# Optimization experiments

Hardware: AMD Instinct MI355X
Metric: run time of the kernel (lower is better)

## Reference

```python
import jax, jax.numpy as jnp
import numpy as np

IMG_H = IMG_W = 14
HEADS = 8
HEAD_DIM = 32
INNER = HEADS * HEAD_DIM  # 256
IN_CH = 384
OUT_CH = 768
HIDDEN = 4 * IN_CH  # 1536
SCALE = HEAD_DIM ** -0.5
EPS = 1e-5


def _relative_index(h, w):
    # static numpy computation, identical to the torch buffer
    yy, xx = np.meshgrid(np.arange(h), np.arange(w), indexing='ij')
    coords = np.stack([yy.ravel(), xx.ravel()])            # [2, N]
    rel = coords[:, :, None] - coords[:, None, :]          # [2, N, N]
    rel[0] += h - 1
    rel[1] += w - 1
    rel[0] *= 2 * w - 1
    return (rel[0] + rel[1]).reshape(-1)                   # [N*N]


def _maxpool3s2p1(x):
    # torch MaxPool2d(3, 2, 1): pad with -inf
    return jax.lax.reduce_window(
        x, -jnp.inf, jax.lax.max,
        window_dimensions=(1, 1, 3, 3),
        window_strides=(1, 1, 2, 2),
        padding=((0, 0), (0, 0), (1, 1), (1, 1)))


def _layernorm(x, g, b):
    mu = jnp.mean(x, axis=-1, keepdims=True)
    var = jnp.mean(jnp.square(x - mu), axis=-1, keepdims=True)
    return (x - mu) * jax.lax.rsqrt(var + EPS) * g + b


def setup_inputs() -> dict:
    key = jax.random.key(0)
    ks = jax.random.split(key, 12)
    s = 0.02
    return {
        'x': jax.random.normal(ks[0], (64, IN_CH, 28, 28), jnp.float32),
        'W_qkv': jax.random.normal(ks[1], (IN_CH, 3 * INNER), jnp.float32) * s,
        'bias_table': jax.random.normal(ks[2], ((2 * IMG_H - 1) * (2 * IMG_W - 1), HEADS), jnp.float32) * s,
        'W_out': jax.random.normal(ks[3], (INNER, OUT_CH), jnp.float32) * s,
        'b_out': jnp.zeros((OUT_CH,), jnp.float32),
        'ln1_g': jnp.ones((IN_CH,), jnp.float32),
        'ln1_b': jnp.zeros((IN_CH,), jnp.float32),
        'ln2_g': jnp.ones((OUT_CH,), jnp.float32),
        'ln2_b': jnp.zeros((OUT_CH,), jnp.float32),
        'W_fc1': jax.random.normal(ks[4], (OUT_CH, HIDDEN), jnp.float32) * s,
        'b_fc1': jnp.zeros((HIDDEN,), jnp.float32),
        'W_fc2': jax.random.normal(ks[5], (HIDDEN, OUT_CH), jnp.float32) * s,
        'b_fc2': jnp.zeros((OUT_CH,), jnp.float32),
        'W_proj': jax.random.normal(ks[6], (OUT_CH, IN_CH), jnp.float32) * s,
    }


def reference(x, W_qkv, bias_table, W_out, b_out, ln1_g, ln1_b, ln2_g, ln2_b,
              W_fc1, b_fc1, W_fc2, b_fc2, W_proj):
    B = x.shape[0]
    N = IMG_H * IMG_W
    rel_idx = jnp.asarray(_relative_index(IMG_H, IMG_W))   # [N*N]

    # --- downsample branch ---
    xp = _maxpool3s2p1(x)                                  # [B, Cin, 14, 14]
    proj = jnp.einsum('bchw,oc->bohw', xp, W_proj)         # 1x1 conv, no bias

    # --- attention branch ---
    xa = _maxpool3s2p1(x)                                  # [B, Cin, 14, 14]
    tokens = xa.reshape(B, IN_CH, N).transpose(0, 2, 1)    # [B, N, Cin]
    tokens = _layernorm(tokens, ln1_g, ln1_b)
    qkv = tokens @ W_qkv                                   # [B, N, 3*INNER]
    q, k, v = jnp.split(qkv, 3, axis=-1)
    def heads(t):
        return t.reshape(B, N, HEADS, HEAD_DIM).transpose(0, 2, 1, 3)  # [B,H,N,D]
    q, k, v = heads(q), heads(k), heads(v)
    dots = jnp.einsum('bhid,bhjd->bhij', q, k) * SCALE     # [B,H,N,N]
    bias = bias_table[rel_idx].reshape(N, N, HEADS).transpose(2, 0, 1)  # [H,N,N]
    attn = jax.nn.softmax(dots + bias[None], axis=-1)
    out = jnp.einsum('bhij,bhjd->bhid', attn, v)           # [B,H,N,D]
    out = out.transpose(0, 2, 1, 3).reshape(B, N, INNER)
    out = out @ W_out + b_out                              # [B, N, Cout]
    attn_map = out.transpose(0, 2, 1).reshape(B, OUT_CH, IMG_H, IMG_W)

    h = proj + attn_map                                    # [B, Cout, 14, 14]

    # --- feed-forward branch ---
    t = h.reshape(B, OUT_CH, N).transpose(0, 2, 1)         # [B, N, Cout]
    t = _layernorm(t, ln2_g, ln2_b)
    t = jax.nn.gelu(t @ W_fc1 + b_fc1, approximate=False)
    t = t @ W_fc2 + b_fc2
    ffn = t.transpose(0, 2, 1).reshape(B, OUT_CH, IMG_H, IMG_W)

    return h + ffn
```

## Files before the change

kernel.cpp:

```cpp
#include <hip/hip_runtime.h>
#include <hip/hip_bf16.h>
#include <cmath>

typedef unsigned short ushortT;
typedef unsigned int u32;
typedef __attribute__((ext_vector_type(8))) short short8;
typedef __attribute__((ext_vector_type(4))) float floatx4;

#define IMG 14
#define NTOK 196
#define BATCH 64
#define M_TOT 12544
#define M_HALF 6272
#define INCH 384
#define OUTCH 768
#define HIDDEN 1536
#define HEADS 8
#define HDIM 32
#define SCALE 0.17677669529663687f

__device__ __forceinline__ float b2f(ushortT u) {
    union { u32 i; float f; } v; v.i = ((u32)u) << 16; return v.f;
}
__device__ __forceinline__ ushortT f2b(float f) {
    union { float f; u32 i; } v; v.f = f;
    u32 r = v.i + 0x7FFFu + ((v.i >> 16) & 1u);
    return (ushortT)(r >> 16);
}

__device__ __forceinline__ void async_ld16(const void* g, void* l) {
    __builtin_amdgcn_global_load_lds(
        (const __attribute__((address_space(1))) u32*)g,
        (__attribute__((address_space(3))) u32*)l, 16, 0, 0);
}

__global__ __launch_bounds__(256) void prep_pool(
    const float* __restrict__ Wqkv, const float* __restrict__ Wout,
    const float* __restrict__ Wfc1, const float* __restrict__ Wfc2,
    const float* __restrict__ Wproj, const float* __restrict__ x,
    const float* __restrict__ bias_tb,
    ushortT* __restrict__ oQkv, ushortT* __restrict__ oOut,
    ushortT* __restrict__ oFc1, ushortT* __restrict__ oFc2,
    ushortT* __restrict__ oProj, ushortT* __restrict__ pooled,
    float* __restrict__ bias_exp) {
    __shared__ __align__(16) char lds_raw[26880];
    int blk = blockIdx.x;
    int tid = threadIdx.x;
    if (blk >= 4608) {
        int idx4 = (blk - 4608) * 256 + tid;
        int h = idx4 / 10816;
        int rem = idx4 - h * 10816;
        int i = rem / 52;
        int j0 = (rem - i * 52) * 4;
        float v[4];
        #pragma unroll
        for (int u = 0; u < 4; ++u) {
            int j = j0 + u;
            float val = 0.f;
            if (i < 196 && j < 196) {
                int iy = i / 14, ix = i - iy * 14;
                int jy = j / 14, jx = j - jy * 14;
                val = bias_tb[((iy - jy + 13) * 27 + (ix - jx + 13)) * 8 + h];
            }
            v[u] = val;
        }
        *(float4*)(bias_exp + (size_t)idx4 * 4) = *(const float4*)v;
        return;
    }
    if (blk >= 3072) {
        int pblk = blk - 3072;
        int cg = pblk % 24, b = pblk / 24;
        float* hm = (float*)lds_raw;
        const float* xsrc = x + ((size_t)b * INCH + cg * 16) * 784;
        for (int t = tid; t < 448; t += 256) {
            int c = t / 28, hrow = t - c * 28;
            const float* rp = xsrc + c * 784 + hrow * 28;
            float r[28];
            #pragma unroll
            for (int u = 0; u < 7; ++u)
                *(float4*)(r + u * 4) = *(const float4*)(rp + u * 4);
            float* hr = hm + (size_t)t * 15;
            #pragma unroll
            for (int j = 0; j < 14; ++j) {
                float a = j ? r[2 * j - 1] : r[0];
                hr[j] = fmaxf(fmaxf(a, r[2 * j]), r[2 * j + 1]);
            }
        }
        __syncthreads();
        for (int chunk = tid; chunk < NTOK * 2; chunk += 256) {
            int n = chunk >> 1, q = chunk & 1;
            int hh = n / IMG, ww = n - hh * IMG;
            int ya = hh ? 2 * hh - 1 : 0;
            int y1 = 2 * hh, y2 = 2 * hh + 1;
            ushortT o[8];
            #pragma unroll
            for (int cc = 0; cc < 8; ++cc) {
                const float* base = hm + (size_t)(q * 8 + cc) * 28 * 15 + ww;
                float mv = fmaxf(fmaxf(base[ya * 15], base[y1 * 15]), base[y2 * 15]);
                o[cc] = f2b(mv);
            }
            *(uint4*)(pooled + ((size_t)b * NTOK + n) * INCH + cg * 16 + q * 8) =
                *(const uint4*)o;
        }
        return;
    }
    if (blk >= 2784) {
        int i = ((blk - 2784) * 256 + tid) * 4;
        float4 v = *(const float4*)(Wproj + i);
        ushortT o[4] = { f2b(v.x), f2b(v.y), f2b(v.z), f2b(v.w) };
        *(uint2*)(oProj + i) = *(const uint2*)o;
        return;
    }
    const float* in; ushortT* out; int R, C, tile;
    if (blk < 288)       { in = Wqkv; out = oQkv; R = 384;  C = 768;  tile = blk; }
    else if (blk < 480)  { in = Wout; out = oOut; R = 256;  C = 768;  tile = blk - 288; }
    else if (blk < 1632) { in = Wfc1; out = oFc1; R = 768;  C = 1536; tile = blk - 480; }
    else                 { in = Wfc2; out = oFc2; R = 1536; C = 768;  tile = blk - 1632; }
    int tilesX = C >> 5;
    int bx = (tile % tilesX) * 32, by = (tile / tilesX) * 32;
    ushortT (*t)[33] = (ushortT (*)[33])lds_raw;
    int tx = tid & 31, ty = tid >> 5;
    #pragma unroll
    for (int i = 0; i < 4; ++i) {
        int r = by + ty * 4 + i;
        t[ty * 4 + i][tx] = f2b(in[(size_t)r * C + bx + tx]);
    }
    __syncthreads();
    #pragma unroll
    for (int i = 0; i < 4; ++i) {
        int r = bx + ty * 4 + i;
        out[(size_t)r * R + by + tx] = t[tx][ty * 4 + i];
    }
}

template <int VE>
__global__ __launch_bounds__(256) void ln_kernel(const ushortT* __restrict__ in,
                                                 const float* __restrict__ gw,
                                                 const float* __restrict__ bw,
                                                 ushortT* __restrict__ out) {
    constexpr int C = 192 * VE;
    int wave = threadIdx.x >> 6, lane = threadIdx.x & 63;
    int m = blockIdx.x * 4 + wave;
    const ushortT* row = in + (size_t)m * C;
    float v[3][VE];
    float s = 0.f, q = 0.f;
    #pragma unroll
    for (int seg = 0; seg < 3; ++seg) {
        int idx = seg * 64 * VE + lane * VE;
        ushortT tmp[VE];
        if constexpr (VE == 2) *(u32*)tmp = *(const u32*)(row + idx);
        else                   *(uint2*)tmp = *(const uint2*)(row + idx);
        #pragma unroll
        for (int k = 0; k < VE; ++k) {
            float f = b2f(tmp[k]);
            v[seg][k] = f;
            s += f;
            q += f * f;
        }
    }
    #pragma unroll
    for (int off = 32; off > 0; off >>= 1) {
        s += __shfl_xor(s, off, 64);
        q += __shfl_xor(q, off, 64);
    }
    float mu = s / (float)C;
    float var = q / (float)C - mu * mu;
    float rs = rsqrtf(var + 1e-5f);
    #pragma unroll
    for (int seg = 0; seg < 3; ++seg) {
        int idx = seg * 64 * VE + lane * VE;
        float g[VE], bb[VE];
        if constexpr (VE == 2) {
            *(float2*)g = *(const float2*)(gw + idx);
            *(float2*)bb = *(const float2*)(bw + idx);
        } else {
            *(float4*)g = *(const float4*)(gw + idx);
            *(float4*)bb = *(const float4*)(bw + idx);
        }
        ushortT o[VE];
        #pragma unroll
        for (int k = 0; k < VE; ++k)
            o[k] = f2b((v[seg][k] - mu) * rs * g[k] + bb[k]);
        if constexpr (VE == 2) *(u32*)(out + (size_t)m * C + idx) = *(const u32*)o;
        else                   *(uint2*)(out + (size_t)m * C + idx) = *(const uint2*)o;
    }
}

__global__ __launch_bounds__(256) void attn_kernel(const ushortT* __restrict__ qkv,
                                                   const float* __restrict__ bias_exp,
                                                   ushortT* __restrict__ attn_out) {
    int bh = blockIdx.x;
    int b = bh >> 3, h = bh & 7;
    __shared__ ushortT Qs[208 * 32];
    __shared__ ushortT Ks[208 * 32];
    __shared__ ushortT Vts[32 * 232];
    __shared__ ushortT Ps[4][16 * 232];
    const int tid = threadIdx.x, wave = tid >> 6, lane = tid & 63;

    const uint4* q4 = (const uint4*)(qkv + (size_t)bh * 6272);
    const uint4* k4 = (const uint4*)(qkv + (size_t)(512 + bh) * 6272);
    const uint4* v4 = (const uint4*)(qkv + (size_t)(1024 + bh) * 6272);
    uint4* Q4 = (uint4*)Qs;
    uint4* K4 = (uint4*)Ks;
    for (int t = tid; t < 784; t += 256) { Q4[t] = q4[t]; K4[t] = k4[t]; }
    const uint4 z4 = {0, 0, 0, 0};
    for (int t = tid; t < 48; t += 256) { Q4[784 + t] = z4; K4[784 + t] = z4; }
    for (int t = tid; t < 784; t += 256) {
        int j = t >> 2, d0 = (t & 3) * 8;
        uint4 v = v4[t];
        const ushortT* vs = (const ushortT*)&v;
        #pragma unroll
        for (int u = 0; u < 8; ++u)
            Vts[(d0 + u) * 232 + j] = vs[u];
    }
    for (int t = tid; t < 1152; t += 256) {
        int d = t / 36, j = 196 + t - d * 36;
        Vts[d * 232 + j] = 0;
    }
    for (int t = tid; t < 1536; t += 256) {
        int w = t / 384, rem = t - w * 384;
        int row = rem / 24, j = 208 + rem - (rem / 24) * 24;
        Ps[w][row * 232 + j] = 0;
    }
    __syncthreads();

    const int fr = (lane & 15), fk = (lane >> 4) * 8;
    short8 kf[13];
    #pragma unroll
    for (int nt = 0; nt < 13; ++nt)
        kf[nt] = *(const short8*)(Ks + (nt * 16 + fr) * 32 + fk);

    const int i0r = (lane >> 4) * 4;
    const int colL = lane & 15;
    ushortT* Pw = &Ps[wave][0];

    for (int mt = wave; mt < 13; mt += 4) {
        short8 af = *(const short8*)(Qs + (mt * 16 + fr) * 32 + fk);
        floatx4 sc[13];
        #pragma unroll
        for (int nt = 0; nt < 13; ++nt)
            sc[nt] = __builtin_amdgcn_mfma_f32_16x16x32_bf16(
                af, kf[nt], (floatx4){0.f, 0.f, 0.f, 0.f}, 0, 0, 0);

        float rsum[4] = {0.f, 0.f, 0.f, 0.f};
        const float* bb = bias_exp + ((size_t)h * 208 + mt * 16 + i0r) * 208 + colL;
        #pragma unroll
        for (int nt = 0; nt < 13; ++nt) {
            #pragma unroll
            for (int r = 0; r < 4; ++r) {
                float bias = bb[r * 208 + nt * 16];
                float p = __expf(sc[nt][r] * SCALE + bias);
                if (nt == 12 && colL >= 4) p = 0.f;
                rsum[r] += p;
                Pw[(i0r + r) * 232 + nt * 16 + colL] = f2b(p);
            }
        }
        #pragma unroll
        for (int off = 1; off < 16; off <<= 1) {
            #pragma unroll
            for (int r = 0; r < 4; ++r) rsum[r] += __shfl_xor(rsum[r], off, 64);
        }

        floatx4 o[2];
        o[0] = (floatx4){0.f, 0.f, 0.f, 0.f};
        o[1] = (floatx4){0.f, 0.f, 0.f, 0.f};
        #pragma unroll
        for (int kt = 0; kt < 7; ++kt) {
            short8 pf = *(const short8*)(Pw + fr * 232 + kt * 32 + fk);
            #pragma unroll
            for (int n2 = 0; n2 < 2; ++n2) {
                short8 vf = *(const short8*)(Vts + (n2 * 16 + fr) * 232 + kt * 32 + fk);
                o[n2] = __builtin_amdgcn_mfma_f32_16x16x32_bf16(pf, vf, o[n2], 0, 0, 0);
            }
        }
        float invl[4];
        #pragma unroll
        for (int r = 0; r < 4; ++r) invl[r] = 1.f / rsum[r];
        #pragma unroll
        for (int n2 = 0; n2 < 2; ++n2) {
            #pragma unroll
            for (int r = 0; r < 4; ++r) {
                int i = mt * 16 + i0r + r;
                if (i < 196)
                    attn_out[((size_t)(b * 196 + i)) * 256 + h * 32 + n2 * 16 + colL] =
                        f2b(o[n2][r] * invl[r]);
            }
        }
    }
}

template <int BN, int EPI, typename OUT_T>
__global__ __launch_bounds__(256) void gemm64(
    const ushortT* __restrict__ A1, const ushortT* __restrict__ B1, int K1,
    const ushortT* __restrict__ A2, const ushortT* __restrict__ B2, int K2,
    const float* __restrict__ bias, const ushortT* __restrict__ addend,
    OUT_T* __restrict__ out, int m_off) {
    __shared__ ushortT As[64 * 32];
    __shared__ ushortT Bs[BN * 32];
    const int tid = threadIdx.x, wave = tid >> 6, lane = tid & 63;
    constexpr int MT = (BN == 128) ? 4 : 2;
    constexpr int NT = 2;
    const int wmo = (BN == 128) ? 0 : (wave & 1) * 32;
    const int wno = (BN == 128) ? wave * 32 : (wave >> 1) * 32;
    const int tm = blockIdx.x, tn = blockIdx.y;

    floatx4 acc[MT][NT];
    #pragma unroll
    for (int a = 0; a < MT; ++a)
        #pragma unroll
        for (int c = 0; c < NT; ++c)
            acc[a][c] = (floatx4){0.f, 0.f, 0.f, 0.f};

    const int glrow = lane >> 2, glcol = (lane & 3) * 8;
    const int kof = (lane >> 4) * 8;

    auto stage = [&](const ushortT* G, int ld, int row0, int k0, ushortT* S, int R16) {
        for (int i = wave; i < R16; i += 4)
            async_ld16(G + (size_t)(row0 + i * 16 + glrow) * ld + k0 + glcol, S + i * 512);
    };

    auto kloop = [&](const ushortT* A, const ushortT* B, int K) {
        for (int k0 = 0; k0 < K; k0 += 32) {
            stage(A, K, tm * 64, k0, As, 4);
            stage(B, K, tn * BN, k0, Bs, BN / 16);
            __syncthreads();
            short8 af[MT], bf[NT];
            #pragma unroll
            for (int mt = 0; mt < MT; ++mt)
                af[mt] = *(const short8*)(As + (wmo + mt * 16 + (lane & 15)) * 32 + kof);
            #pragma unroll
            for (int nt = 0; nt < NT; ++nt)
                bf[nt] = *(const short8*)(Bs + (wno + nt * 16 + (lane & 15)) * 32 + kof);
            #pragma unroll
            for (int mt = 0; mt < MT; ++mt)
                #pragma unroll
                for (int nt = 0; nt < NT; ++nt)
                    acc[mt][nt] = __builtin_amdgcn_mfma_f32_16x16x32_bf16(
                        af[mt], bf[nt], acc[mt][nt], 0, 0, 0);
            __syncthreads();
        }
    };

    kloop(A1, B1, K1);
    if (B2) kloop(A2, B2, K2);

    const int nb = tn * BN + wno + (lane & 15);
    const int mbl = wmo + ((lane >> 4) << 2);
    #pragma unroll
    for (int nt = 0; nt < NT; ++nt) {
        int n = nb + nt * 16;
        float bv = (EPI == 0) ? 0.f : bias[n];
        #pragma unroll
        for (int mt = 0; mt < MT; ++mt) {
            #pragma unroll
            for (int r = 0; r < 4; ++r) {
                int m = tm * 64 + mbl + mt * 16 + r;
                float v = acc[mt][nt][r] + bv;
                if constexpr (EPI == 0) {
                    int bb = m / 196, tok = m - bb * 196;
                    int reg = n >> 8, head = (n >> 5) & 7, d = n & 31;
                    out[((size_t)((reg * 512 + bb * 8 + head) * 196 + tok)) * 32 + d] = f2b(v);
                } else if constexpr (EPI == 1) {
                    out[(size_t)m * 768 + n] = f2b(v);
                } else if constexpr (EPI == 2) {
                    float gl = 0.5f * v * (1.f + erff(v * 0.70710678118654752f));
                    out[(size_t)m * 1536 + n] = f2b(gl);
                } else {
                    v += b2f(addend[(size_t)m * 768 + n]);
                    int mg = m + m_off;
                    int bb = mg / 196, tok = mg - bb * 196;
                    out[((size_t)(bb * 768 + n)) * 196 + tok] = v;
                }
            }
        }
    }
}

extern "C" void kernel_launch(void* const* d_in, const int* in_sizes, int n_in,
                              void* d_out, int out_size, void* d_ws, size_t ws_size,
                              hipStream_t stream) {
    const float* x       = (const float*)d_in[0];
    const float* W_qkv   = (const float*)d_in[1];
    const float* bias_tb = (const float*)d_in[2];
    const float* W_out   = (const float*)d_in[3];
    const float* b_out   = (const float*)d_in[4];
    const float* ln1_g   = (const float*)d_in[5];
    const float* ln1_b   = (const float*)d_in[6];
    const float* ln2_g   = (const float*)d_in[7];
    const float* ln2_b   = (const float*)d_in[8];
    const float* W_fc1   = (const float*)d_in[9];
    const float* b_fc1   = (const float*)d_in[10];
    const float* W_fc2   = (const float*)d_in[11];
    const float* b_fc2   = (const float*)d_in[12];
    const float* W_proj  = (const float*)d_in[13];
    float* out = (float*)d_out;

    char* ws = (char*)d_ws;
    ushortT* pooled = (ushortT*)(ws);
    ushortT* tln1   = (ushortT*)(ws + 9633792);
    ushortT* attno  = tln1;
    ushortT* qkvb   = (ushortT*)(ws + 19267584);
    ushortT* tln2   = qkvb;
    ushortT* mid    = (ushortT*)(ws);
    ushortT* htok   = (ushortT*)(ws + 38535168);
    float*   bias_exp = (float*)(ws + 38535168);
    ushortT* wTqkv  = (ushortT*)(ws + 57802752);
    ushortT* wTout  = wTqkv + 768 * 384;
    ushortT* wTfc1  = wTout + 768 * 256;
    ushortT* wTfc2  = wTfc1 + 1536 * 768;
    ushortT* wProjB = wTfc2 + 768 * 1536;

    prep_pool<<<4946, 256, 0, stream>>>(W_qkv, W_out, W_fc1, W_fc2, W_proj, x, bias_tb,
                                        wTqkv, wTout, wTfc1, wTfc2, wProjB, pooled,
                                        bias_exp);

    ln_kernel<2><<<M_TOT / 4, 256, 0, stream>>>(pooled, ln1_g, ln1_b, tln1);

    gemm64<128, 0, ushortT><<<dim3(196, 6), 256, 0, stream>>>(tln1, wTqkv, 384,
                                                nullptr, nullptr, 0,
                                                nullptr, nullptr, qkvb, 0);
    attn_kernel<<<512, 256, 0, stream>>>(qkvb, bias_exp, attno);

    gemm64<128, 1, ushortT><<<dim3(196, 6), 256, 0, stream>>>(attno, wTout, 256,
                                                pooled, wProjB, 384,
                                                b_out, nullptr, htok, 0);
    ln_kernel<4><<<M_TOT / 4, 256, 0, stream>>>(htok, ln2_g, ln2_b, tln2);

    for (int half = 0; half < 2; ++half) {
        const ushortT* a2 = tln2 + (size_t)half * M_HALF * 768;
        gemm64<128, 2, ushortT><<<dim3(98, 12), 256, 0, stream>>>(a2, wTfc1, 768,
                                                     nullptr, nullptr, 0,
                                                     b_fc1, nullptr, mid, 0);
        gemm64<64, 3, float><<<dim3(98, 12), 256, 0, stream>>>(mid, wTfc2, 1536,
                                                    nullptr, nullptr, 0,
                                                    b_fc2, htok + (size_t)half * M_HALF * 768,
                                                    out, half * M_HALF);
    }
    (void)in_sizes; (void)n_in; (void)out_size; (void)ws_size;
}
```

Before: 409.3 us.

## Enlarge GEMM tiles to 128x128 and run FFN in one pass when workspace allows

Replaces the 64-row GEMM kernel with a 128x128 tile kernel in which each of the four waves computes a 64x64 sub-tile with 4x4 MFMA accumulators. This raises MFMA work per LDS load and per barrier. When the workspace is large enough, the FFN now runs as a single fc1 and a single fc2 launch over all tokens, using a separate full-size intermediate buffer instead of two halves. The larger tiles need more registers and give fewer blocks, which may lower occupancy on the smaller grids.

```diff
diff --git a/kernel.cpp b/kernel.cpp
--- a/kernel.cpp
+++ b/kernel.cpp
@@ -289,52 +289,52 @@
     }
 }
 
-template <int BN, int EPI, typename OUT_T>
-__global__ __launch_bounds__(256) void gemm64(
+template <int EPI, typename OUT_T>
+__global__ __launch_bounds__(256) void gemm128(
     const ushortT* __restrict__ A1, const ushortT* __restrict__ B1, int K1,
     const ushortT* __restrict__ A2, const ushortT* __restrict__ B2, int K2,
     const float* __restrict__ bias, const ushortT* __restrict__ addend,
     OUT_T* __restrict__ out, int m_off) {
-    __shared__ ushortT As[64 * 32];
-    __shared__ ushortT Bs[BN * 32];
+    __shared__ ushortT As[128 * 32];
+    __shared__ ushortT Bs[128 * 32];
     const int tid = threadIdx.x, wave = tid >> 6, lane = tid & 63;
-    constexpr int MT = (BN == 128) ? 4 : 2;
-    constexpr int NT = 2;
-    const int wmo = (BN == 128) ? 0 : (wave & 1) * 32;
-    const int wno = (BN == 128) ? wave * 32 : (wave >> 1) * 32;
+    const int wr = (wave >> 1) * 64;
+    const int wc = (wave & 1) * 64;
     const int tm = blockIdx.x, tn = blockIdx.y;
 
-    floatx4 acc[MT][NT];
-    #pragma unroll
-    for (int a = 0; a < MT; ++a)
-        #pragma unroll
-        for (int c = 0; c < NT; ++c)
+    floatx4 acc[4][4];
+    #pragma unroll
+    for (int a = 0; a < 4; ++a)
+        #pragma unroll
+        for (int c = 0; c < 4; ++c)
             acc[a][c] = (floatx4){0.f, 0.f, 0.f, 0.f};
 
-    const int glrow = lane >> 2, glcol = (lane & 3) * 8;
-    const int kof = (lane >> 4) * 8;
-
-    auto stage = [&](const ushortT* G, int ld, int row0, int k0, ushortT* S, int R16) {
-        for (int i = wave; i < R16; i += 4)
-            async_ld16(G + (size_t)(row0 + i * 16 + glrow) * ld + k0 + glcol, S + i * 512);
+    const int fr = lane & 15, fk = (lane >> 4) * 8;
+
+    auto stage = [&](const ushortT* G, int ld, int row0, int k0, ushortT* S) {
+        #pragma unroll
+        for (int i = 0; i < 2; ++i) {
+            int c = tid + i * 256;
+            async_ld16(G + (size_t)(row0 + (c >> 2)) * ld + k0 + (c & 3) * 8, S + c * 8);
+        }
     };
 
     auto kloop = [&](const ushortT* A, const ushortT* B, int K) {
         for (int k0 = 0; k0 < K; k0 += 32) {
-            stage(A, K, tm * 64, k0, As, 4);
-            stage(B, K, tn * BN, k0, Bs, BN / 16);
+            stage(A, K, tm * 128, k0, As);
+            stage(B, K, tn * 128, k0, Bs);
             __syncthreads();
-            short8 af[MT], bf[NT];
-            #pragma unroll
-            for (int mt = 0; mt < MT; ++mt)
-                af[mt] = *(const short8*)(As + (wmo + mt * 16 + (lane & 15)) * 32 + kof);
-            #pragma unroll
-            for (int nt = 0; nt < NT; ++nt)
-                bf[nt] = *(const short8*)(Bs + (wno + nt * 16 + (lane & 15)) * 32 + kof);
-            #pragma unroll
-            for (int mt = 0; mt < MT; ++mt)
+            short8 af[4], bf[4];
+            #pragma unroll
+            for (int mt = 0; mt < 4; ++mt)
+                af[mt] = *(const short8*)(As + (wr + mt * 16 + fr) * 32 + fk);
+            #pragma unroll
+            for (int nt = 0; nt < 4; ++nt)
+                bf[nt] = *(const short8*)(Bs + (wc + nt * 16 + fr) * 32 + fk);
+            #pragma unroll
+            for (int mt = 0; mt < 4; ++mt)
                 #pragma unroll
-                for (int nt = 0; nt < NT; ++nt)
+                for (int nt = 0; nt < 4; ++nt)
                     acc[mt][nt] = __builtin_amdgcn_mfma_f32_16x16x32_bf16(
                         af[mt], bf[nt], acc[mt][nt], 0, 0, 0);
             __syncthreads();
@@ -344,17 +344,17 @@
     kloop(A1, B1, K1);
     if (B2) kloop(A2, B2, K2);
 
-    const int nb = tn * BN + wno + (lane & 15);
-    const int mbl = wmo + ((lane >> 4) << 2);
-    #pragma unroll
-    for (int nt = 0; nt < NT; ++nt) {
+    const int nb = tn * 128 + wc + (lane & 15);
+    const int mbl = wr + ((lane >> 4) << 2);
+    #pragma unroll
+    for (int nt = 0; nt < 4; ++nt) {
         int n = nb + nt * 16;
         float bv = (EPI == 0) ? 0.f : bias[n];
         #pragma unroll
-        for (int mt = 0; mt < MT; ++mt) {
+        for (int mt = 0; mt < 4; ++mt) {
             #pragma unroll
             for (int r = 0; r < 4; ++r) {
-                int m = tm * 64 + mbl + mt * 16 + r;
+                int m = tm * 128 + mbl + mt * 16 + r;
                 float v = acc[mt][nt][r] + bv;
                 if constexpr (EPI == 0) {
                     int bb = m / 196, tok = m - bb * 196;
@@ -409,6 +409,10 @@
     ushortT* wTfc1  = wTout + 768 * 256;
     ushortT* wTfc2  = wTfc1 + 1536 * 768;
     ushortT* wProjB = wTfc2 + 768 * 1536;
+    const size_t weights_end = 57802752 +
+        (size_t)(768 * 384 + 768 * 256 + 1536 * 768 + 768 * 1536 + 768 * 384) * 2;
+    const bool ffn_full = ws_size >= weights_end + (size_t)M_TOT * HIDDEN * 2;
+    ushortT* midf = (ushortT*)(ws + weights_end);
 
     prep_pool<<<4946, 256, 0, stream>>>(W_qkv, W_out, W_fc1, W_fc2, W_proj, x, bias_tb,
                                         wTqkv, wTout, wTfc1, wTfc2, wProjB, pooled,
@@ -416,25 +420,34 @@
 
     ln_kernel<2><<<M_TOT / 4, 256, 0, stream>>>(pooled, ln1_g, ln1_b, tln1);
 
-    gemm64<128, 0, ushortT><<<dim3(196, 6), 256, 0, stream>>>(tln1, wTqkv, 384,
+    gemm128<0, ushortT><<<dim3(98, 6), 256, 0, stream>>>(tln1, wTqkv, 384,
                                                 nullptr, nullptr, 0,
                                                 nullptr, nullptr, qkvb, 0);
     attn_kernel<<<512, 256, 0, stream>>>(qkvb, bias_exp, attno);
 
-    gemm64<128, 1, ushortT><<<dim3(196, 6), 256, 0, stream>>>(attno, wTout, 256,
+    gemm128<1, ushortT><<<dim3(98, 6), 256, 0, stream>>>(attno, wTout, 256,
                                                 pooled, wProjB, 384,
                                                 b_out, nullptr, htok, 0);
     ln_kernel<4><<<M_TOT / 4, 256, 0, stream>>>(htok, ln2_g, ln2_b, tln2);
 
-    for (int half = 0; half < 2; ++half) {
-        const ushortT* a2 = tln2 + (size_t)half * M_HALF * 768;
-        gemm64<128, 2, ushortT><<<dim3(98, 12), 256, 0, stream>>>(a2, wTfc1, 768,
+    if (ffn_full) {
+        gemm128<2, ushortT><<<dim3(98, 12), 256, 0, stream>>>(tln2, wTfc1, 768,
                                                      nullptr, nullptr, 0,
-                                                     b_fc1, nullptr, mid, 0);
-        gemm64<64, 3, float><<<dim3(98, 12), 256, 0, stream>>>(mid, wTfc2, 1536,
+                                                     b_fc1, nullptr, midf, 0);
+        gemm128<3, float><<<dim3(98, 6), 256, 0, stream>>>(midf, wTfc2, 1536,
                                                     nullptr, nullptr, 0,
-                                                    b_fc2, htok + (size_t)half * M_HALF * 768,
-                                                    out, half * M_HALF);
+                                                    b_fc2, htok, out, 0);
+    } else {
+        for (int half = 0; half < 2; ++half) {
+            const ushortT* a2 = tln2 + (size_t)half * M_HALF * 768;
+            gemm128<2, ushortT><<<dim3(49, 12), 256, 0, stream>>>(a2, wTfc1, 768,
+                                                         nullptr, nullptr, 0,
+                                                         b_fc1, nullptr, mid, 0);
+            gemm128<3, float><<<dim3(49, 6), 256, 0, stream>>>(mid, wTfc2, 1536,
+                                                        nullptr, nullptr, 0,
+                                                        b_fc2, htok + (size_t)half * M_HALF * 768,
+                                                        out, half * M_HALF);
+        }
     }
     (void)in_sizes; (void)n_in; (void)out_size; (void)ws_size;
 }
```

Result: slower. 422.5 us (+3.2%).
